# Kernel tuning notes

Hardware: AMD Instinct MI355X
Metric: run time of the kernel (lower is better)

The kernel has to match this reference:

```python
import jax, jax.numpy as jnp
import numpy as np

N = 200000   # active voxels
G = 128      # dense grid extent per axis
C = 128      # hidden channels
IN_C = 1
TEMB = 6
K = 27       # 3x3x3 kernel offsets


def _build_neighbors():
    # Sample N unique voxel coordinates in a G^3 grid and build the 27-offset
    # rulebook: neighbor_idx[k, i] = index of voxel at coord[i] + offset[k],
    # or N (sentinel -> zero-padded feature row) if inactive.
    rng = np.random.default_rng(0)
    lin = np.sort(rng.choice(G ** 3, size=N, replace=False)).astype(np.int64)
    x, r = lin // (G * G), lin % (G * G)
    y, z = r // G, r % G
    nidx = np.full((K, N), N, dtype=np.int32)
    k = 0
    for dx in (-1, 0, 1):
        for dy in (-1, 0, 1):
            for dz in (-1, 0, 1):
                nx, ny, nz = x + dx, y + dy, z + dz
                valid = (nx >= 0) & (nx < G) & (ny >= 0) & (ny < G) & (nz >= 0) & (nz < G)
                key = nx * (G * G) + ny * G + nz
                pos = np.searchsorted(lin, key)
                posc = np.clip(pos, 0, N - 1)
                found = valid & (lin[posc] == key)
                nidx[k] = np.where(found, posc, N).astype(np.int32)
                k += 1
    return jnp.asarray(nidx)


def setup_inputs() -> dict:
    key = jax.random.key(0)
    ks = jax.random.split(key, 8)
    s = jnp.float32(0.05)
    return {
        "features": jax.random.normal(ks[0], (N, IN_C), jnp.float32),
        "t": jax.random.randint(ks[1], (N,), 0, 1000, jnp.int32),
        "neighbor_idx": _build_neighbors(),
        "W1": jax.random.normal(ks[2], (K, IN_C + TEMB, C), jnp.float32) * s,
        "b1": jnp.zeros((C,), jnp.float32),
        "W2": jax.random.normal(ks[3], (K, C, C), jnp.float32) * s,
        "b2": jnp.zeros((C,), jnp.float32),
        "W3": jax.random.normal(ks[4], (C, C), jnp.float32) * s,
        "b3": jnp.zeros((C,), jnp.float32),
        "W4": jax.random.normal(ks[5], (C, 1), jnp.float32) * s,
        "b4": jnp.zeros((1,), jnp.float32),
    }


def _sinusoidal(t, dim):
    half = dim // 2
    freqs = (2.0 ** jnp.arange(half, dtype=jnp.float32)) * jnp.pi  # 2^k * pi
    ang = t.astype(jnp.float32)[:, None] * freqs[None, :]
    return jnp.concatenate([jnp.sin(ang), jnp.cos(ang)], -1)  # [N, dim]


def _sparse_conv3(x, W, b, nidx):
    # Submanifold sparse 3x3x3 conv: for each of 27 offsets, gather neighbor
    # features (zero row for missing) and accumulate a [Cin,Cout] matmul.
    xpad = jnp.concatenate([x, jnp.zeros((1, x.shape[1]), x.dtype)], 0)  # sentinel row
    acc0 = jnp.zeros((x.shape[0], W.shape[-1]), x.dtype)

    def step(acc, kw):
        idx, Wk = kw
        return acc + xpad[idx] @ Wk, None

    acc, _ = jax.lax.scan(step, acc0, (nidx, W))
    return acc + b


def reference(features, t, neighbor_idx, W1, b1, W2, b2, W3, b3, W4, b4):
    # time-embedding concat  [N, 1+6]
    x = jnp.concatenate([features, _sinusoidal(t, TEMB)], -1)
    # SparseConv3d(k=3) + Dropout(eval: identity) + SiLU
    h = jax.nn.silu(_sparse_conv3(x, W1, b1, neighbor_idx))
    h = jax.nn.silu(_sparse_conv3(h, W2, b2, neighbor_idx))
    # SparseConv3d(k=1) + SiLU  == pointwise matmul
    h = jax.nn.silu(h @ W3 + b3)
    # final 1x1 conv to out_channels=1
    return h @ W4 + b4
```

## Files before the change

### kernel.cpp

```cpp
#include <hip/hip_runtime.h>
#include <math.h>

#define N_VOX 200000
#define CCH   128
#define KOFF  27

typedef __attribute__((ext_vector_type(8))) short bf16x8;
typedef __attribute__((ext_vector_type(4))) float f32x4;

__device__ __forceinline__ float silu_f(float x) {
    return x / (1.0f + expf(-x));
}
__device__ __forceinline__ unsigned short f2bf(float x) {
    unsigned int u = __float_as_uint(x);
    u = (u + 0x7FFFu + ((u >> 16) & 1u)) >> 16;
    return (unsigned short)u;
}
__device__ __forceinline__ int xcd_swz(int orig, int nwg) {
    int q = nwg >> 3, r = nwg & 7;
    int xcd = orig & 7, pos = orig >> 3;
    return (xcd < r ? xcd * (q + 1) : r * (q + 1) + (xcd - r) * q) + pos;
}

__global__ void embed_kernel(const float* __restrict__ feat,
                             const int* __restrict__ t,
                             unsigned short* __restrict__ xeb) {
    int i = blockIdx.x * blockDim.x + threadIdx.x;
    if (i > N_VOX) return;
    union { unsigned short u[8]; int4 v; } o;
    if (i == N_VOX) {
        o.v = make_int4(0, 0, 0, 0);
    } else {
        o.u[0] = f2bf(feat[i]);
        float tf = (float)t[i];
#pragma unroll
        for (int kk = 0; kk < 3; ++kk) {
            float freq = (float)M_PI * (float)(1 << kk);
            float ang = tf * freq;
            o.u[1 + kk] = f2bf(sinf(ang));
            o.u[4 + kk] = f2bf(cosf(ang));
        }
        o.u[7] = 0;
    }
    *(int4*)(xeb + (size_t)i * 8) = o.v;
}

__global__ void convert_w1(const float* __restrict__ W1,
                           unsigned short* __restrict__ W1f) {
    int g = blockIdx.x * 256 + threadIdx.x;
    if (g >= 7 * 8 * 64) return;
    int l = g & 63;
    int rest = g >> 6;
    int nf = rest & 7;
    int kk = rest >> 3;
    int o = kk * 4 + (l >> 4);
    int co = nf * 16 + (l & 15);
    union { unsigned short u[8]; int4 v; } out;
#pragma unroll
    for (int j = 0; j < 8; ++j) {
        float w = 0.f;
        if (o < KOFF && j < 7) w = W1[((size_t)o * 7 + j) * CCH + co];
        out.u[j] = f2bf(w);
    }
    *(int4*)(W1f + (size_t)g * 8) = out.v;
}

__global__ void convert_w2(const float* __restrict__ W2,
                           unsigned short* __restrict__ W2f) {
    int g = blockIdx.x * 256 + threadIdx.x;
    int l = g & 63;
    int rest = g >> 6;
    int nf = rest & 7;
    int kkk = rest >> 3;
    int k = kkk >> 2, kk = kkk & 3;
    int ci0 = kk * 32 + (l >> 4) * 8;
    int co = nf * 16 + (l & 15);
    union { unsigned short u[8]; int4 v; } out;
#pragma unroll
    for (int j = 0; j < 8; ++j)
        out.u[j] = f2bf(W2[((size_t)k * CCH + ci0 + j) * CCH + co]);
    *(int4*)(W2f + (size_t)g * 8) = out.v;
}

__global__ void convert_w3(const float* __restrict__ W3,
                           unsigned short* __restrict__ W3f) {
    int g = blockIdx.x * 256 + threadIdx.x;
    if (g >= 4 * 8 * 64) return;
    int l = g & 63;
    int rest = g >> 6;
    int nf = rest & 7;
    int kk = rest >> 3;
    int ci0 = kk * 32 + (l >> 4) * 8;
    int co = nf * 16 + (l & 15);
    union { unsigned short u[8]; int4 v; } out;
#pragma unroll
    for (int j = 0; j < 8; ++j)
        out.u[j] = f2bf(W3[(size_t)(ci0 + j) * CCH + co]);
    *(int4*)(W3f + (size_t)g * 8) = out.v;
}

__global__ __launch_bounds__(256) void conv1_mfma(
    const unsigned short* __restrict__ xeb, const int* __restrict__ nidx,
    const unsigned short* __restrict__ W1f, const float* __restrict__ b1,
    unsigned short* __restrict__ h1b) {
    __shared__ int4 bufmem[2048];
    __shared__ int idxAll[128 * 28];

    int tid = threadIdx.x;
    int l = tid & 63, w = tid >> 6;
    int mw = w >> 1, nwv = w & 1;
    int wg = xcd_swz(blockIdx.x, gridDim.x);
    int v0 = wg * 128;

    for (int g = tid; g < KOFF * 128; g += 256) {
        int k = g >> 7, vi = g & 127;
        int v = v0 + vi;
        idxAll[vi * 28 + k] = (v < N_VOX) ? nidx[(size_t)k * N_VOX + v] : N_VOX;
    }
    if (tid < 128) idxAll[tid * 28 + 27] = N_VOX;
    __syncthreads();

    f32x4 acc[4][4];
#pragma unroll
    for (int m = 0; m < 4; ++m)
#pragma unroll
        for (int n = 0; n < 4; ++n) acc[m][n] = (f32x4)0.f;

    {
        int4 g0[2]; int rr[2], cc[2];
#pragma unroll
        for (int u = 0; u < 2; ++u) {
            int q = u * 256 + tid;
            int r = q >> 2, oo = q & 3;
            int idx = idxAll[r * 28 + oo];
            g0[u] = *(const int4*)(xeb + (size_t)idx * 8);
            rr[u] = r; cc[u] = oo ^ (r & 3);
        }
#pragma unroll
        for (int u = 0; u < 2; ++u) bufmem[rr[u] * 5 + cc[u]] = g0[u];
    }
    __syncthreads();

    for (int kk = 0; kk < 7; ++kk) {
        int cur = kk & 1;
        int4 gg[2]; int rr[2], cc[2];
        if (kk < 6) {
#pragma unroll
            for (int u = 0; u < 2; ++u) {
                int q = u * 256 + tid;
                int r = q >> 2, oo = q & 3;
                int idx = idxAll[r * 28 + (kk + 1) * 4 + oo];
                gg[u] = *(const int4*)(xeb + (size_t)idx * 8);
                rr[u] = r; cc[u] = oo ^ (r & 3);
            }
        }
        bf16x8 a[4], b[4];
#pragma unroll
        for (int n = 0; n < 4; ++n) {
            int nf = nwv * 4 + n;
            b[n] = *(const bf16x8*)(W1f + ((size_t)(kk * 8 + nf) * 64 + l) * 8);
        }
#pragma unroll
        for (int m = 0; m < 4; ++m) {
            int r = mw * 64 + m * 16 + (l & 15);
            int c = l >> 4;
            a[m] = *(const bf16x8*)&bufmem[cur * 640 + r * 5 + (c ^ (r & 3))];
        }
#pragma unroll
        for (int m = 0; m < 4; ++m)
#pragma unroll
            for (int n = 0; n < 4; ++n)
                acc[m][n] = __builtin_amdgcn_mfma_f32_16x16x32_bf16(
                    a[m], b[n], acc[m][n], 0, 0, 0);
        if (kk < 6) {
#pragma unroll
            for (int u = 0; u < 2; ++u)
                bufmem[(cur ^ 1) * 640 + rr[u] * 5 + cc[u]] = gg[u];
        }
        __syncthreads();
    }

    float bias[4];
#pragma unroll
    for (int n = 0; n < 4; ++n) bias[n] = b1[nwv * 64 + n * 16 + (l & 15)];
    unsigned short* H16 = (unsigned short*)bufmem;
#pragma unroll
    for (int m = 0; m < 4; ++m) {
        int rbase = mw * 64 + m * 16 + (l >> 4) * 4;
#pragma unroll
        for (int n = 0; n < 4; ++n) {
            int ch = nwv * 64 + n * 16 + (l & 15);
            int c = ch >> 3;
            f32x4 d = acc[m][n];
#pragma unroll
            for (int ri = 0; ri < 4; ++ri) {
                int r = rbase + ri;
                int s = (c & 8) | ((c & 7) ^ (r & 7));
                H16[r * 128 + s * 8 + (ch & 7)] = f2bf(silu_f(d[ri] + bias[n]));
            }
        }
    }
    __syncthreads();
#pragma unroll
    for (int u = 0; u < 8; ++u) {
        int q = u * 256 + tid;
        int r = q >> 4, s = q & 15;
        int c = (s & 8) | ((s & 7) ^ (r & 7));
        int v = v0 + r;
        if (v < N_VOX)
            *(int4*)(h1b + (size_t)v * CCH + c * 8) = bufmem[r * 16 + s];
    }
    if (blockIdx.x == 0 && tid < 16)
        *(int4*)(h1b + (size_t)N_VOX * CCH + tid * 8) = make_int4(0, 0, 0, 0);
}

__global__ __launch_bounds__(256, 4) void conv2_mfma(
    const unsigned short* __restrict__ h1b, const int* __restrict__ nidx,
    const unsigned short* __restrict__ W2f, const float* __restrict__ b2,
    const unsigned short* __restrict__ W3f, const float* __restrict__ b3,
    const float* __restrict__ W4, const float* __restrict__ b4,
    float* __restrict__ out) {
    __shared__ int4 Abuf[2][64 * 16];
    __shared__ int idxAll[28 * 64];

    int tid = threadIdx.x;
    int l = tid & 63, w = tid >> 6;
    int mw = w >> 1, nwv = w & 1;
    int wg = xcd_swz(blockIdx.x, gridDim.x);
    int v0 = wg * 64;

    for (int g = tid; g < KOFF * 64; g += 256) {
        int k = g >> 6, vi = g & 63;
        int v = v0 + vi;
        idxAll[k * 64 + vi] = (v < N_VOX) ? nidx[(size_t)k * N_VOX + v] : N_VOX;
    }
    __syncthreads();

    f32x4 acc[2][4];
#pragma unroll
    for (int m = 0; m < 2; ++m)
#pragma unroll
        for (int n = 0; n < 4; ++n) acc[m][n] = (f32x4)0.f;

    {
        int4 g0[4];
#pragma unroll
        for (int u = 0; u < 4; ++u) {
            int q = u * 256 + tid;
            int r = q >> 4, s = q & 15;
            int c = (s & 8) | ((s & 7) ^ (r & 7));
            int idx = idxAll[r];
            g0[u] = *(const int4*)(h1b + (size_t)idx * CCH + c * 8);
        }
#pragma unroll
        for (int u = 0; u < 4; ++u) {
            int q = u * 256 + tid;
            Abuf[0][(q >> 4) * 16 + (q & 15)] = g0[u];
        }
    }
    __syncthreads();

    for (int k = 0; k < KOFF; ++k) {
        int cur = k & 1;
        size_t base = (size_t)k * 4 * 8 * 64 * 8;
        bf16x8 bA[4], bB[4];
#pragma unroll
        for (int n = 0; n < 4; ++n) {
            int nf = nwv * 4 + n;
            bA[n] = *(const bf16x8*)(W2f + base + ((size_t)(0 * 8 + nf) * 64 + l) * 8);
            bB[n] = *(const bf16x8*)(W2f + base + ((size_t)(1 * 8 + nf) * 64 + l) * 8);
        }
        int4 gg[4];
        if (k + 1 < KOFF) {
#pragma unroll
            for (int u = 0; u < 4; ++u) {
                int q = u * 256 + tid;
                int r = q >> 4, s = q & 15;
                int c = (s & 8) | ((s & 7) ^ (r & 7));
                int idx = idxAll[(k + 1) * 64 + r];
                gg[u] = *(const int4*)(h1b + (size_t)idx * CCH + c * 8);
            }
        }
#pragma unroll
        for (int kk = 0; kk < 2; ++kk) {
            bf16x8 a[2];
#pragma unroll
            for (int m = 0; m < 2; ++m) {
                int r = mw * 32 + m * 16 + (l & 15);
                int c = kk * 4 + (l >> 4);
                int s = (c & 8) | ((c & 7) ^ (r & 7));
                a[m] = *(const bf16x8*)&Abuf[cur][r * 16 + s];
            }
            bf16x8* bb = kk ? bB : bA;
#pragma unroll
            for (int m = 0; m < 2; ++m)
#pragma unroll
                for (int n = 0; n < 4; ++n)
                    acc[m][n] = __builtin_amdgcn_mfma_f32_16x16x32_bf16(
                        a[m], bb[n], acc[m][n], 0, 0, 0);
        }
#pragma unroll
        for (int n = 0; n < 4; ++n) {
            int nf = nwv * 4 + n;
            bA[n] = *(const bf16x8*)(W2f + base + ((size_t)(2 * 8 + nf) * 64 + l) * 8);
            bB[n] = *(const bf16x8*)(W2f + base + ((size_t)(3 * 8 + nf) * 64 + l) * 8);
        }
#pragma unroll
        for (int kk = 2; kk < 4; ++kk) {
            bf16x8 a[2];
#pragma unroll
            for (int m = 0; m < 2; ++m) {
                int r = mw * 32 + m * 16 + (l & 15);
                int c = kk * 4 + (l >> 4);
                int s = (c & 8) | ((c & 7) ^ (r & 7));
                a[m] = *(const bf16x8*)&Abuf[cur][r * 16 + s];
            }
            bf16x8* bb = (kk == 3) ? bB : bA;
#pragma unroll
            for (int m = 0; m < 2; ++m)
#pragma unroll
                for (int n = 0; n < 4; ++n)
                    acc[m][n] = __builtin_amdgcn_mfma_f32_16x16x32_bf16(
                        a[m], bb[n], acc[m][n], 0, 0, 0);
        }
        if (k + 1 < KOFF) {
#pragma unroll
            for (int u = 0; u < 4; ++u) {
                int q = u * 256 + tid;
                Abuf[cur ^ 1][(q >> 4) * 16 + (q & 15)] = gg[u];
            }
        }
        __syncthreads();
    }

    float bias2[4];
#pragma unroll
    for (int n = 0; n < 4; ++n) bias2[n] = b2[nwv * 64 + n * 16 + (l & 15)];
    unsigned short* H16 = (unsigned short*)&Abuf[0][0];
#pragma unroll
    for (int m = 0; m < 2; ++m) {
        int rbase = mw * 32 + m * 16 + (l >> 4) * 4;
#pragma unroll
        for (int n = 0; n < 4; ++n) {
            int ch = nwv * 64 + n * 16 + (l & 15);
            int c = ch >> 3;
            f32x4 d = acc[m][n];
#pragma unroll
            for (int ri = 0; ri < 4; ++ri) {
                int r = rbase + ri;
                int s = (c & 8) | ((c & 7) ^ (r & 7));
                H16[r * 128 + s * 8 + (ch & 7)] = f2bf(silu_f(d[ri] + bias2[n]));
            }
        }
    }
    __syncthreads();

    f32x4 p[2][4];
#pragma unroll
    for (int m = 0; m < 2; ++m)
#pragma unroll
        for (int n = 0; n < 4; ++n) p[m][n] = (f32x4)0.f;
#pragma unroll
    for (int kk = 0; kk < 4; ++kk) {
        bf16x8 a[2], b[4];
#pragma unroll
        for (int n = 0; n < 4; ++n) {
            int nf = nwv * 4 + n;
            b[n] = *(const bf16x8*)(W3f + ((size_t)(kk * 8 + nf) * 64 + l) * 8);
        }
#pragma unroll
        for (int m = 0; m < 2; ++m) {
            int r = mw * 32 + m * 16 + (l & 15);
            int c = kk * 4 + (l >> 4);
            int s = (c & 8) | ((c & 7) ^ (r & 7));
            a[m] = *(const bf16x8*)&Abuf[0][r * 16 + s];
        }
#pragma unroll
        for (int m = 0; m < 2; ++m)
#pragma unroll
            for (int n = 0; n < 4; ++n)
                p[m][n] = __builtin_amdgcn_mfma_f32_16x16x32_bf16(
                    a[m], b[n], p[m][n], 0, 0, 0);
    }

    float w4v[4], b3v[4];
#pragma unroll
    for (int n = 0; n < 4; ++n) {
        int ch = nwv * 64 + n * 16 + (l & 15);
        w4v[n] = W4[ch];
        b3v[n] = b3[ch];
    }
    float* Osum = (float*)idxAll;
#pragma unroll
    for (int m = 0; m < 2; ++m) {
        float po[4] = {0.f, 0.f, 0.f, 0.f};
#pragma unroll
        for (int n = 0; n < 4; ++n) {
            f32x4 d = p[m][n];
#pragma unroll
            for (int ri = 0; ri < 4; ++ri)
                po[ri] += silu_f(d[ri] + b3v[n]) * w4v[n];
        }
#pragma unroll
        for (int off = 1; off < 16; off <<= 1)
#pragma unroll
            for (int ri = 0; ri < 4; ++ri)
                po[ri] += __shfl_xor(po[ri], off, 64);
        if ((l & 15) == 0) {
            int rbase = mw * 32 + m * 16 + (l >> 4) * 4;
#pragma unroll
            for (int ri = 0; ri < 4; ++ri)
                Osum[nwv * 64 + rbase + ri] = po[ri];
        }
    }
    __syncthreads();
    if (tid < 64) {
        int v = v0 + tid;
        if (v < N_VOX) out[v] = Osum[tid] + Osum[64 + tid] + b4[0];
    }
}

extern "C" void kernel_launch(void* const* d_in, const int* in_sizes, int n_in,
                              void* d_out, int out_size, void* d_ws,
                              size_t ws_size, hipStream_t stream) {
    const float* feat = (const float*)d_in[0];
    const int* t      = (const int*)d_in[1];
    const int* nidx   = (const int*)d_in[2];
    const float* W1   = (const float*)d_in[3];
    const float* b1   = (const float*)d_in[4];
    const float* W2   = (const float*)d_in[5];
    const float* b2   = (const float*)d_in[6];
    const float* W3   = (const float*)d_in[7];
    const float* b3   = (const float*)d_in[8];
    const float* W4   = (const float*)d_in[9];
    const float* b4   = (const float*)d_in[10];
    float* out = (float*)d_out;

    char* ws = (char*)d_ws;
    size_t off = 0;
    unsigned short* xeb = (unsigned short*)(ws + off);
    off += ((size_t)(N_VOX + 1) * 8 * 2 + 255) & ~(size_t)255;
    unsigned short* h1b = (unsigned short*)(ws + off);
    off += ((size_t)(N_VOX + 1) * CCH * 2 + 255) & ~(size_t)255;
    unsigned short* W1f = (unsigned short*)(ws + off);
    off += ((size_t)7 * 8 * 64 * 8 * 2 + 255) & ~(size_t)255;
    unsigned short* W2f = (unsigned short*)(ws + off);
    off += ((size_t)KOFF * 4 * 8 * 64 * 8 * 2 + 255) & ~(size_t)255;
    unsigned short* W3f = (unsigned short*)(ws + off);

    int grid1 = (N_VOX + 127) / 128;
    int grid2 = (N_VOX + 63) / 64;
    embed_kernel<<<(N_VOX + 1 + 255) / 256, 256, 0, stream>>>(feat, t, xeb);
    convert_w1<<<(7 * 8 * 64 + 255) / 256, 256, 0, stream>>>(W1, W1f);
    convert_w2<<<(KOFF * 4 * 8 * 64) / 256, 256, 0, stream>>>(W2, W2f);
    convert_w3<<<(4 * 8 * 64 + 255) / 256, 256, 0, stream>>>(W3, W3f);
    conv1_mfma<<<grid1, 256, 0, stream>>>(xeb, nidx, W1f, b1, h1b);
    conv2_mfma<<<grid2, 256, 0, stream>>>(h1b, nidx, W2f, b2, W3f, b3, W4, b4, out);
}
```

Baseline: 296.3 us.

## Gather conv2 A fragments straight into registers with register double-buffering

The conv2 main loop no longer stages gathered neighbor rows through a double-buffered LDS tile with a barrier per offset. Each wave now loads its own MFMA A fragments directly from global memory into registers, prefetching the next offset's fragments while the current MFMAs run. A sentinel index row is added so the final prefetch stays in bounds. This removes 27 block barriers and the LDS write/read round trip, but the two N-half waves now fetch the same rows twice, and register pressure rises, so occupancy is lowered to 3 blocks.

```diff
diff --git a/kernel.cpp b/kernel.cpp
--- a/kernel.cpp
+++ b/kernel.cpp
@@ -214,14 +214,58 @@
         *(int4*)(h1b + (size_t)N_VOX * CCH + tid * 8) = make_int4(0, 0, 0, 0);
 }
 
-__global__ __launch_bounds__(256, 4) void conv2_mfma(
+#define LOAD_A(dst, kq) {                                                  \
+    int _i0 = idxp[(kq) * 64];                                             \
+    int _i1 = idxp[(kq) * 64 + 16];                                        \
+    int _o0 = (_i0 << 8) + lane_c16;                                       \
+    int _o1 = (_i1 << 8) + lane_c16;                                       \
+    const char* _h = (const char*)h1b;                                     \
+    dst[0][0] = *(const bf16x8*)(_h + _o0);                                \
+    dst[0][1] = *(const bf16x8*)(_h + _o0 + 64);                           \
+    dst[0][2] = *(const bf16x8*)(_h + _o0 + 128);                          \
+    dst[0][3] = *(const bf16x8*)(_h + _o0 + 192);                          \
+    dst[1][0] = *(const bf16x8*)(_h + _o1);                                \
+    dst[1][1] = *(const bf16x8*)(_h + _o1 + 64);                           \
+    dst[1][2] = *(const bf16x8*)(_h + _o1 + 128);                         \
+    dst[1][3] = *(const bf16x8*)(_h + _o1 + 192);                          \
+}
+
+#define BODY(KQ, AC, AN) {                                                 \
+    const unsigned short* _wb = W2f + (size_t)(KQ) * 16384;                \
+    bf16x8 _b0[4], _b1[4];                                                 \
+    _Pragma("unroll") for (int n = 0; n < 4; ++n) {                        \
+        int nf = nwv * 4 + n;                                              \
+        _b0[n] = *(const bf16x8*)(_wb + ((0 * 8 + nf) * 64 + l) * 8);      \
+        _b1[n] = *(const bf16x8*)(_wb + ((1 * 8 + nf) * 64 + l) * 8);      \
+    }                                                                      \
+    LOAD_A(AN, (KQ) + 1);                                                  \
+    _Pragma("unroll") for (int n = 0; n < 4; ++n) {                        \
+        acc[0][n] = __builtin_amdgcn_mfma_f32_16x16x32_bf16(AC[0][0], _b0[n], acc[0][n], 0, 0, 0); \
+        acc[1][n] = __builtin_amdgcn_mfma_f32_16x16x32_bf16(AC[1][0], _b0[n], acc[1][n], 0, 0, 0); \
+        acc[0][n] = __builtin_amdgcn_mfma_f32_16x16x32_bf16(AC[0][1], _b1[n], acc[0][n], 0, 0, 0); \
+        acc[1][n] = __builtin_amdgcn_mfma_f32_16x16x32_bf16(AC[1][1], _b1[n], acc[1][n], 0, 0, 0); \
+    }                                                                      \
+    _Pragma("unroll") for (int n = 0; n < 4; ++n) {                        \
+        int nf = nwv * 4 + n;                                              \
+        _b0[n] = *(const bf16x8*)(_wb + ((2 * 8 + nf) * 64 + l) * 8);      \
+        _b1[n] = *(const bf16x8*)(_wb + ((3 * 8 + nf) * 64 + l) * 8);      \
+    }                                                                      \
+    _Pragma("unroll") for (int n = 0; n < 4; ++n) {                        \
+        acc[0][n] = __builtin_amdgcn_mfma_f32_16x16x32_bf16(AC[0][2], _b0[n], acc[0][n], 0, 0, 0); \
+        acc[1][n] = __builtin_amdgcn_mfma_f32_16x16x32_bf16(AC[1][2], _b0[n], acc[1][n], 0, 0, 0); \
+        acc[0][n] = __builtin_amdgcn_mfma_f32_16x16x32_bf16(AC[0][3], _b1[n], acc[0][n], 0, 0, 0); \
+        acc[1][n] = __builtin_amdgcn_mfma_f32_16x16x32_bf16(AC[1][3], _b1[n], acc[1][n], 0, 0, 0); \
+    }                                                                      \
+}
+
+__global__ __launch_bounds__(256, 3) void conv2_mfma(
     const unsigned short* __restrict__ h1b, const int* __restrict__ nidx,
     const unsigned short* __restrict__ W2f, const float* __restrict__ b2,
     const unsigned short* __restrict__ W3f, const float* __restrict__ b3,
     const float* __restrict__ W4, const float* __restrict__ b4,
     float* __restrict__ out) {
-    __shared__ int4 Abuf[2][64 * 16];
     __shared__ int idxAll[28 * 64];
+    __shared__ unsigned short H16[64 * 128];
 
     int tid = threadIdx.x;
     int l = tid & 63, w = tid >> 6;
@@ -232,8 +276,9 @@
     for (int g = tid; g < KOFF * 64; g += 256) {
         int k = g >> 6, vi = g & 63;
         int v = v0 + vi;
-        idxAll[k * 64 + vi] = (v < N_VOX) ? nidx[(size_t)k * N_VOX + v] : N_VOX;
-    }
+        idxAll[g] = (v < N_VOX) ? nidx[(size_t)k * N_VOX + v] : N_VOX;
+    }
+    if (tid < 64) idxAll[KOFF * 64 + tid] = N_VOX;
     __syncthreads();
 
     f32x4 acc[2][4];
@@ -242,101 +287,21 @@
 #pragma unroll
         for (int n = 0; n < 4; ++n) acc[m][n] = (f32x4)0.f;
 
-    {
-        int4 g0[4];
-#pragma unroll
-        for (int u = 0; u < 4; ++u) {
-            int q = u * 256 + tid;
-            int r = q >> 4, s = q & 15;
-            int c = (s & 8) | ((s & 7) ^ (r & 7));
-            int idx = idxAll[r];
-            g0[u] = *(const int4*)(h1b + (size_t)idx * CCH + c * 8);
-        }
-#pragma unroll
-        for (int u = 0; u < 4; ++u) {
-            int q = u * 256 + tid;
-            Abuf[0][(q >> 4) * 16 + (q & 15)] = g0[u];
-        }
-    }
-    __syncthreads();
-
-    for (int k = 0; k < KOFF; ++k) {
-        int cur = k & 1;
-        size_t base = (size_t)k * 4 * 8 * 64 * 8;
-        bf16x8 bA[4], bB[4];
-#pragma unroll
-        for (int n = 0; n < 4; ++n) {
-            int nf = nwv * 4 + n;
-            bA[n] = *(const bf16x8*)(W2f + base + ((size_t)(0 * 8 + nf) * 64 + l) * 8);
-            bB[n] = *(const bf16x8*)(W2f + base + ((size_t)(1 * 8 + nf) * 64 + l) * 8);
-        }
-        int4 gg[4];
-        if (k + 1 < KOFF) {
-#pragma unroll
-            for (int u = 0; u < 4; ++u) {
-                int q = u * 256 + tid;
-                int r = q >> 4, s = q & 15;
-                int c = (s & 8) | ((s & 7) ^ (r & 7));
-                int idx = idxAll[(k + 1) * 64 + r];
-                gg[u] = *(const int4*)(h1b + (size_t)idx * CCH + c * 8);
-            }
-        }
-#pragma unroll
-        for (int kk = 0; kk < 2; ++kk) {
-            bf16x8 a[2];
-#pragma unroll
-            for (int m = 0; m < 2; ++m) {
-                int r = mw * 32 + m * 16 + (l & 15);
-                int c = kk * 4 + (l >> 4);
-                int s = (c & 8) | ((c & 7) ^ (r & 7));
-                a[m] = *(const bf16x8*)&Abuf[cur][r * 16 + s];
-            }
-            bf16x8* bb = kk ? bB : bA;
-#pragma unroll
-            for (int m = 0; m < 2; ++m)
-#pragma unroll
-                for (int n = 0; n < 4; ++n)
-                    acc[m][n] = __builtin_amdgcn_mfma_f32_16x16x32_bf16(
-                        a[m], bb[n], acc[m][n], 0, 0, 0);
-        }
-#pragma unroll
-        for (int n = 0; n < 4; ++n) {
-            int nf = nwv * 4 + n;
-            bA[n] = *(const bf16x8*)(W2f + base + ((size_t)(2 * 8 + nf) * 64 + l) * 8);
-            bB[n] = *(const bf16x8*)(W2f + base + ((size_t)(3 * 8 + nf) * 64 + l) * 8);
-        }
-#pragma unroll
-        for (int kk = 2; kk < 4; ++kk) {
-            bf16x8 a[2];
-#pragma unroll
-            for (int m = 0; m < 2; ++m) {
-                int r = mw * 32 + m * 16 + (l & 15);
-                int c = kk * 4 + (l >> 4);
-                int s = (c & 8) | ((c & 7) ^ (r & 7));
-                a[m] = *(const bf16x8*)&Abuf[cur][r * 16 + s];
-            }
-            bf16x8* bb = (kk == 3) ? bB : bA;
-#pragma unroll
-            for (int m = 0; m < 2; ++m)
-#pragma unroll
-                for (int n = 0; n < 4; ++n)
-                    acc[m][n] = __builtin_amdgcn_mfma_f32_16x16x32_bf16(
-                        a[m], bb[n], acc[m][n], 0, 0, 0);
-        }
-        if (k + 1 < KOFF) {
-#pragma unroll
-            for (int u = 0; u < 4; ++u) {
-                int q = u * 256 + tid;
-                Abuf[cur ^ 1][(q >> 4) * 16 + (q & 15)] = gg[u];
-            }
-        }
-        __syncthreads();
-    }
+    int vi0 = mw * 32 + (l & 15);
+    const int* idxp = &idxAll[vi0];
+    int lane_c16 = (l >> 4) * 16;
+
+    bf16x8 aE[2][4], aO[2][4];
+    LOAD_A(aE, 0);
+    for (int k = 0; k < 26; k += 2) {
+        BODY(k, aE, aO);
+        BODY(k + 1, aO, aE);
+    }
+    BODY(26, aE, aO);
 
     float bias2[4];
 #pragma unroll
     for (int n = 0; n < 4; ++n) bias2[n] = b2[nwv * 64 + n * 16 + (l & 15)];
-    unsigned short* H16 = (unsigned short*)&Abuf[0][0];
 #pragma unroll
     for (int m = 0; m < 2; ++m) {
         int rbase = mw * 32 + m * 16 + (l >> 4) * 4;
@@ -373,7 +338,7 @@
             int r = mw * 32 + m * 16 + (l & 15);
             int c = kk * 4 + (l >> 4);
             int s = (c & 8) | ((c & 7) ^ (r & 7));
-            a[m] = *(const bf16x8*)&Abuf[0][r * 16 + s];
+            a[m] = *(const bf16x8*)&H16[r * 128 + s * 8];
         }
 #pragma unroll
         for (int m = 0; m < 2; ++m)
```

After: 363.8 us. +22.8%, slower.
